# Kernel optimization log

Hardware: AMD Instinct MI355X
Metric: run time of the kernel (lower is better)

## Reference

```python
import jax, jax.numpy as jnp
import numpy as np

WS = 8        # world_size (tp group size)
M = 8192      # global M, divisible by WS
N = 4096
LOCAL_K = 1024  # K // WS


def setup_inputs() -> dict:
    key = jax.random.key(0)
    k1, k2 = jax.random.split(key)
    # Per-rank K-sharded activation and weight (transpose_weight=False => weight is [N, local_K])
    inp = jax.random.normal(k1, (WS, M, LOCAL_K), dtype=jnp.float32)
    wgt = jax.random.normal(k2, (WS, N, LOCAL_K), dtype=jnp.float32) * 0.02
    return {"input": inp, "weight": wgt}


def reference(input, weight):
    """GEMM + reduce-scatter across the TP group.

    Each rank r computes partial_r = input[r] @ weight[r].T  -> [M, N].
    Reduce: full = sum_r partial_r. Scatter: rank r receives rows
    [r*M/WS : (r+1)*M/WS]. We return the scattered result for all ranks
    stacked on the leading axis: [WS, M//WS, N].
    """
    # Contract over both the rank axis (the reduce) and local_K in one einsum.
    full = jnp.einsum('rmk,rnk->mn', input, weight)  # [M, N]
    return full.reshape(WS, M // WS, N)
```

## Files before the change

### kernel.cpp

```cpp
#include <hip/hip_runtime.h>
#include <hip/hip_bf16.h>


#define M_TOT 8192
#define N_TOT 4096
#define LK    1024
#define NR    8
#define K_TOT (NR * LK)
#define NT    (K_TOT / 64)

typedef float f32x4 __attribute__((ext_vector_type(4)));
typedef short s16x8 __attribute__((ext_vector_type(8)));
typedef const __attribute__((address_space(1))) unsigned int* gptr_t;
typedef __attribute__((address_space(3))) unsigned int* lptr_t;

__device__ inline short f2bf(float f) {
    __hip_bfloat16 h = __float2bfloat16(f);
    return *reinterpret_cast<short*>(&h);
}

__global__ __launch_bounds__(256)
void cvt_bf16(const float* __restrict__ in, short* __restrict__ out,
              int row_shift, int row_mask) {
    const int row = blockIdx.x * 2 + (threadIdx.x >> 7);
    const int c   = (threadIdx.x & 127) * 8;
    const int r   = row >> row_shift;
    const int m   = row & row_mask;
    const float* src = in + ((size_t)row << 10) + c;
    f32x4 v0 = *(const f32x4*)src;
    f32x4 v1 = *(const f32x4*)(src + 4);
    s16x8 o;
    #pragma unroll
    for (int j = 0; j < 4; ++j) { o[j] = f2bf(v0[j]); o[j + 4] = f2bf(v1[j]); }
    *(s16x8*)(out + ((size_t)m << 13) + ((size_t)r << 10) + c) = o;
}


__device__ __forceinline__ void stage_half(const short* srcBase, short* ldsOp,
                                           int half, int ktile, int wid) {
    #pragma unroll
    for (int q = 0; q < 2; ++q) {
        const short* src = srcBase + (size_t)(half * 128 + q * 8) * K_TOT + ktile * 64;
        short* dst = ldsOp + (half * 128 + wid * 16 + q * 8) * 64;
        __builtin_amdgcn_global_load_lds((gptr_t)src, (lptr_t)dst, 16, 0, 0);
    }
}

template<int C>
__device__ __forceinline__ void read_a_pair(s16x8 (&afr)[8][2], const short* lAc,
                                            int wm, int r15, int kg) {
    #pragma unroll
    for (int fo = 0; fo < 2; ++fo)
        #pragma unroll
        for (int ks = 0; ks < 2; ++ks) {
            const int row = C * 64 + wm * 32 + fo * 16 + r15;
            const int off = row * 64 + ((((ks << 2) | kg) ^ (row & 7)) << 3);
            afr[C * 2 + fo][ks] = *(const s16x8*)(lAc + off);
        }
}

__device__ __forceinline__ void read_b(s16x8 (&bfr)[4][2], const short* lBc,
                                       int wn, int r15, int kg) {
    #pragma unroll
    for (int n = 0; n < 4; ++n)
        #pragma unroll
        for (int ks = 0; ks < 2; ++ks) {
            const int row = wn * 64 + n * 16 + r15;
            const int off = row * 64 + ((((ks << 2) | kg) ^ (row & 7)) << 3);
            bfr[n][ks] = *(const s16x8*)(lBc + off);
        }
}

template<int Q>
__device__ __forceinline__ void mfma_quad(f32x4 (&acc)[8][4], s16x8 (&afr)[8][2],
                                          s16x8 (&bfr)[4][2]) {
    __builtin_amdgcn_s_setprio(1);
    #pragma unroll
    for (int fo = 0; fo < 2; ++fo)
        #pragma unroll
        for (int n = 0; n < 4; ++n)
            #pragma unroll
            for (int ks = 0; ks < 2; ++ks)
                acc[Q * 2 + fo][n] = __builtin_amdgcn_mfma_f32_16x16x32_bf16(
                    afr[Q * 2 + fo][ks], bfr[n][ks], acc[Q * 2 + fo][n], 0, 0, 0);
    __builtin_amdgcn_s_setprio(0);
}

#define MEMCLOB asm volatile("" ::: "memory")
#define BAR     __builtin_amdgcn_s_barrier()
#define SCHED0  __builtin_amdgcn_sched_barrier(0)

#define TILE_BODY(P) do {                                                     \
    const int t = 2 * t2 + (P);                                               \
    const short* lAc = smem + ((P) << 15);                                    \
    short* bufN = smem + (((P) ^ 1) << 15);                                   \
    short* bufC = smem + ((P) << 15);                                         \
                                             \
    read_a_pair<1>(afr, lAc, wm, r15, kg);                                    \
    if (t + 1 < NT) stage_half(srcA, bufN, 1, t + 1, wid);                    \
    MEMCLOB; BAR;                                                             \
    asm volatile("s_waitcnt lgkmcnt(4)" ::: "memory"); SCHED0;                \
    mfma_quad<0>(acc, afr, bfr);                                              \
    MEMCLOB; BAR;                                                             \
         \
    read_a_pair<2>(afr, lAc, wm, r15, kg);                                    \
    if (t + 2 < NT) stage_half(srcB, bufC + 16384, 0, t + 2, wid);            \
    MEMCLOB; BAR;                                                             \
    asm volatile("s_waitcnt lgkmcnt(4)" ::: "memory"); SCHED0;                \
    mfma_quad<1>(acc, afr, bfr);                                              \
    MEMCLOB; BAR;                                                             \
                                             \
    read_a_pair<3>(afr, lAc, wm, r15, kg);                                    \
    if (t + 2 < NT) stage_half(srcB, bufC + 16384, 1, t + 2, wid);            \
    MEMCLOB; BAR;                                                             \
    asm volatile("s_waitcnt lgkmcnt(4)" ::: "memory"); SCHED0;                \
    mfma_quad<2>(acc, afr, bfr);                                              \
    MEMCLOB; BAR;                                                             \
    \
    \
    \
    \
    asm volatile("s_waitcnt lgkmcnt(0)" ::: "memory");                        \
    if (t < NT - 2)       asm volatile("s_waitcnt vmcnt(4)" ::: "memory");    \
    else if (t == NT - 2) asm volatile("s_waitcnt vmcnt(0)" ::: "memory");    \
    MEMCLOB; BAR; SCHED0;                                                     \
    mfma_quad<3>(acc, afr, bfr);                                              \
    if (t + 1 < NT) {                                                         \
        read_b(bfr, bufN + 16384, wn, r15, kg);                               \
        read_a_pair<0>(afr, bufN, wm, r15, kg);                               \
    }                                                                         \
    if (t + 2 < NT) stage_half(srcA, bufC, 0, t + 2, wid);                    \
    MEMCLOB; BAR;                                                             \
} while (0)

__global__ __launch_bounds__(512, 2)
void gemm8(const short* __restrict__ A, const short* __restrict__ B,
           float* __restrict__ C) {
    extern __shared__ short smem[];

    const int tid  = threadIdx.x;
    const int lane = tid & 63;
    const int wid  = tid >> 6;
    const int wm   = wid >> 2;
    const int wn   = wid & 3;
    const int r15  = lane & 15;
    const int kg   = lane >> 4;
    const int l8   = lane >> 3;
    const int g16  = (lane & 7) ^ l8;

    const int bid = blockIdx.x;
    const int sw  = (bid & 7) * 64 + (bid >> 3);
    const int bm  = sw >> 4;
    const int bn  = sw & 15;

    const short* srcA = A + (size_t)(bm * 256 + wid * 16 + l8) * K_TOT + g16 * 8;
    const short* srcB = B + (size_t)(bn * 256 + wid * 16 + l8) * K_TOT + g16 * 8;

    stage_half(srcB, smem + 16384, 0, 0, wid);
    stage_half(srcB, smem + 16384, 1, 0, wid);
    stage_half(srcA, smem,         0, 0, wid);
    stage_half(srcA, smem,         1, 0, wid);
    stage_half(srcB, smem + 49152, 0, 1, wid);
    stage_half(srcB, smem + 49152, 1, 1, wid);
    stage_half(srcA, smem + 32768, 0, 1, wid);
    asm volatile("s_waitcnt vmcnt(6)" ::: "memory");
    MEMCLOB; BAR;

    f32x4 acc[8][4];
    #pragma unroll
    for (int f = 0; f < 8; ++f)
        #pragma unroll
        for (int n = 0; n < 4; ++n)
            acc[f][n] = (f32x4){0.f, 0.f, 0.f, 0.f};

    s16x8 afr[8][2];
    s16x8 bfr[4][2];

    read_b(bfr, smem + 16384, wn, r15, kg);
    read_a_pair<0>(afr, smem, wm, r15, kg);

    for (int t2 = 0; t2 < NT / 2; ++t2) {
        TILE_BODY(0);
        TILE_BODY(1);
    }

    float* Cp = C + (size_t)(bm * 256 + wm * 32 + kg * 4) * N_TOT
                  + bn * 256 + wn * 64 + r15;
    #pragma unroll
    for (int f = 0; f < 8; ++f)
        #pragma unroll
        for (int n = 0; n < 4; ++n)
            #pragma unroll
            for (int jj = 0; jj < 4; ++jj) {
                const int roff = (f >> 1) * 64 + (f & 1) * 16 + jj;
                Cp[(size_t)roff * N_TOT + n * 16] = acc[f][n][jj];
            }
}

#define PAD_ROW 40
__global__ __launch_bounds__(256, 2)
void gemm_rs_fused(const float* __restrict__ A, const float* __restrict__ B,
                   float* __restrict__ C) {
    __shared__ short lA[128 * PAD_ROW];
    __shared__ short lB[128 * PAD_ROW];
    const int bid = blockIdx.x;
    const int sw  = (bid & 7) * (int)(gridDim.x >> 3) + (bid >> 3);
    const int bm = sw >> 5, bn = sw & 31;
    const int tid = threadIdx.x, lane = tid & 63, wid = tid >> 6;
    const int wr = wid >> 1, wc = wid & 1, r15 = lane & 15, kg = lane >> 4;
    const int srow = tid >> 1, scg = tid & 1;
    const float* gA = A + ((size_t)(bm * 128 + srow) << 10) + scg * 16;
    const float* gB = B + ((size_t)(bn * 128 + srow) << 10) + scg * 16;
    short* wpA = lA + srow * PAD_ROW + scg * 16;
    short* wpB = lB + srow * PAD_ROW + scg * 16;
    const short* rpA = lA + (wr * 64 + r15) * PAD_ROW + kg * 8;
    const short* rpB = lB + (wc * 64 + r15) * PAD_ROW + kg * 8;
    f32x4 acc[4][4];
    #pragma unroll
    for (int i = 0; i < 4; ++i)
        #pragma unroll
        for (int j = 0; j < 4; ++j) acc[i][j] = (f32x4){0.f, 0.f, 0.f, 0.f};
    for (int t = 0; t < K_TOT / 32; ++t) {
        const int r = t >> 5, k0 = (t & 31) << 5;
        const float* pA = gA + (size_t)r * (M_TOT * LK) + k0;
        const float* pB = gB + (size_t)r * (N_TOT * LK) + k0;
        f32x4 va[4], vb[4];
        #pragma unroll
        for (int q = 0; q < 4; ++q) va[q] = *(const f32x4*)(pA + q * 4);
        #pragma unroll
        for (int q = 0; q < 4; ++q) vb[q] = *(const f32x4*)(pB + q * 4);
        __syncthreads();
        s16x8 oa0, oa1, ob0, ob1;
        #pragma unroll
        for (int q = 0; q < 2; ++q)
            #pragma unroll
            for (int i = 0; i < 4; ++i) {
                oa0[q * 4 + i] = f2bf(va[q][i]);
                oa1[q * 4 + i] = f2bf(va[q + 2][i]);
                ob0[q * 4 + i] = f2bf(vb[q][i]);
                ob1[q * 4 + i] = f2bf(vb[q + 2][i]);
            }
        *(s16x8*)(wpA) = oa0; *(s16x8*)(wpA + 8) = oa1;
        *(s16x8*)(wpB) = ob0; *(s16x8*)(wpB + 8) = ob1;
        __syncthreads();
        s16x8 af[4], bfr2[4];
        #pragma unroll
        for (int i = 0; i < 4; ++i) af[i]   = *(const s16x8*)(rpA + i * 16 * PAD_ROW);
        #pragma unroll
        for (int i = 0; i < 4; ++i) bfr2[i] = *(const s16x8*)(rpB + i * 16 * PAD_ROW);
        #pragma unroll
        for (int i = 0; i < 4; ++i)
            #pragma unroll
            for (int j = 0; j < 4; ++j)
                acc[i][j] = __builtin_amdgcn_mfma_f32_16x16x32_bf16(
                    af[i], bfr2[j], acc[i][j], 0, 0, 0);
    }
    float* Cp = C + (size_t)(bm * 128 + wr * 64 + kg * 4) * N_TOT
                  + bn * 128 + wc * 64 + r15;
    #pragma unroll
    for (int i = 0; i < 4; ++i)
        #pragma unroll
        for (int j = 0; j < 4; ++j)
            #pragma unroll
            for (int jj = 0; jj < 4; ++jj)
                Cp[(size_t)(i * 16 + jj) * N_TOT + j * 16] = acc[i][j][jj];
}

extern "C" void kernel_launch(void* const* d_in, const int* in_sizes, int n_in,
                              void* d_out, int out_size, void* d_ws, size_t ws_size,
                              hipStream_t stream) {
    const float* A = (const float*)d_in[0];
    const float* B = (const float*)d_in[1];
    float* C = (float*)d_out;

    const size_t needA = (size_t)M_TOT * K_TOT * 2;
    const size_t needB = (size_t)N_TOT * K_TOT * 2;

    if (ws_size >= needA + needB) {
        short* Abf = (short*)d_ws;
        short* Bbf = (short*)((char*)d_ws + needA);
        cvt_bf16<<<dim3(NR * M_TOT / 2), dim3(256), 0, stream>>>(A, Abf, 13, 8191);
        cvt_bf16<<<dim3(NR * N_TOT / 2), dim3(256), 0, stream>>>(B, Bbf, 12, 4095);
        gemm8<<<dim3((M_TOT / 256) * (N_TOT / 256)), dim3(512), 131072, stream>>>(Abf, Bbf, C);
    } else {
        gemm_rs_fused<<<dim3((M_TOT / 128) * (N_TOT / 128)), dim3(256), 0, stream>>>(A, B, C);
    }
}
```

Baseline: 523.4 us.

## Replace ping-pong tile macro with simple double-buffered K loop

Removes the hand-interleaved two-tile TILE_BODY schedule, which spread global-to-LDS staging across sub-phases with many barriers. In its place is a plain loop: wait for all loads, one barrier, read fragments, issue the whole next tile's prefetch, then run four MFMA quads with partial LDS waits. The A-fragment register array shrinks to two slots and launch bounds drop to one block per CU, freeing registers. This cuts barrier count and code complexity, but the full vmcnt(0) wait each iteration limits how much global latency overlaps with compute.

```diff
diff --git a/kernel.cpp b/kernel.cpp
--- a/kernel.cpp
+++ b/kernel.cpp
@@ -47,7 +47,7 @@
 }
 
 template<int C>
-__device__ __forceinline__ void read_a_pair(s16x8 (&afr)[8][2], const short* lAc,
+__device__ __forceinline__ void read_a_pair(s16x8 (&afr)[2][2][2], const short* lAc,
                                             int wm, int r15, int kg) {
     #pragma unroll
     for (int fo = 0; fo < 2; ++fo)
@@ -55,7 +55,7 @@
         for (int ks = 0; ks < 2; ++ks) {
             const int row = C * 64 + wm * 32 + fo * 16 + r15;
             const int off = row * 64 + ((((ks << 2) | kg) ^ (row & 7)) << 3);
-            afr[C * 2 + fo][ks] = *(const s16x8*)(lAc + off);
+            afr[C & 1][fo][ks] = *(const s16x8*)(lAc + off);
         }
 }
 
@@ -72,7 +72,7 @@
 }
 
 template<int Q>
-__device__ __forceinline__ void mfma_quad(f32x4 (&acc)[8][4], s16x8 (&afr)[8][2],
+__device__ __forceinline__ void mfma_quad(f32x4 (&acc)[8][4], s16x8 (&afr)[2][2][2],
                                           s16x8 (&bfr)[4][2]) {
     __builtin_amdgcn_s_setprio(1);
     #pragma unroll
@@ -82,7 +82,7 @@
             #pragma unroll
             for (int ks = 0; ks < 2; ++ks)
                 acc[Q * 2 + fo][n] = __builtin_amdgcn_mfma_f32_16x16x32_bf16(
-                    afr[Q * 2 + fo][ks], bfr[n][ks], acc[Q * 2 + fo][n], 0, 0, 0);
+                    afr[Q & 1][fo][ks], bfr[n][ks], acc[Q * 2 + fo][n], 0, 0, 0);
     __builtin_amdgcn_s_setprio(0);
 }
 
@@ -90,50 +90,7 @@
 #define BAR     __builtin_amdgcn_s_barrier()
 #define SCHED0  __builtin_amdgcn_sched_barrier(0)
 
-#define TILE_BODY(P) do {                                                     \
-    const int t = 2 * t2 + (P);                                               \
-    const short* lAc = smem + ((P) << 15);                                    \
-    short* bufN = smem + (((P) ^ 1) << 15);                                   \
-    short* bufC = smem + ((P) << 15);                                         \
-                                             \
-    read_a_pair<1>(afr, lAc, wm, r15, kg);                                    \
-    if (t + 1 < NT) stage_half(srcA, bufN, 1, t + 1, wid);                    \
-    MEMCLOB; BAR;                                                             \
-    asm volatile("s_waitcnt lgkmcnt(4)" ::: "memory"); SCHED0;                \
-    mfma_quad<0>(acc, afr, bfr);                                              \
-    MEMCLOB; BAR;                                                             \
-         \
-    read_a_pair<2>(afr, lAc, wm, r15, kg);                                    \
-    if (t + 2 < NT) stage_half(srcB, bufC + 16384, 0, t + 2, wid);            \
-    MEMCLOB; BAR;                                                             \
-    asm volatile("s_waitcnt lgkmcnt(4)" ::: "memory"); SCHED0;                \
-    mfma_quad<1>(acc, afr, bfr);                                              \
-    MEMCLOB; BAR;                                                             \
-                                             \
-    read_a_pair<3>(afr, lAc, wm, r15, kg);                                    \
-    if (t + 2 < NT) stage_half(srcB, bufC + 16384, 1, t + 2, wid);            \
-    MEMCLOB; BAR;                                                             \
-    asm volatile("s_waitcnt lgkmcnt(4)" ::: "memory"); SCHED0;                \
-    mfma_quad<2>(acc, afr, bfr);                                              \
-    MEMCLOB; BAR;                                                             \
-    \
-    \
-    \
-    \
-    asm volatile("s_waitcnt lgkmcnt(0)" ::: "memory");                        \
-    if (t < NT - 2)       asm volatile("s_waitcnt vmcnt(4)" ::: "memory");    \
-    else if (t == NT - 2) asm volatile("s_waitcnt vmcnt(0)" ::: "memory");    \
-    MEMCLOB; BAR; SCHED0;                                                     \
-    mfma_quad<3>(acc, afr, bfr);                                              \
-    if (t + 1 < NT) {                                                         \
-        read_b(bfr, bufN + 16384, wn, r15, kg);                               \
-        read_a_pair<0>(afr, bufN, wm, r15, kg);                               \
-    }                                                                         \
-    if (t + 2 < NT) stage_half(srcA, bufC, 0, t + 2, wid);                    \
-    MEMCLOB; BAR;                                                             \
-} while (0)
-
-__global__ __launch_bounds__(512, 2)
+__global__ __launch_bounds__(512, 1)
 void gemm8(const short* __restrict__ A, const short* __restrict__ B,
            float* __restrict__ C) {
     extern __shared__ short smem[];
@@ -160,11 +117,6 @@
     stage_half(srcB, smem + 16384, 1, 0, wid);
     stage_half(srcA, smem,         0, 0, wid);
     stage_half(srcA, smem,         1, 0, wid);
-    stage_half(srcB, smem + 49152, 0, 1, wid);
-    stage_half(srcB, smem + 49152, 1, 1, wid);
-    stage_half(srcA, smem + 32768, 0, 1, wid);
-    asm volatile("s_waitcnt vmcnt(6)" ::: "memory");
-    MEMCLOB; BAR;
 
     f32x4 acc[8][4];
     #pragma unroll
@@ -173,15 +125,39 @@
         for (int n = 0; n < 4; ++n)
             acc[f][n] = (f32x4){0.f, 0.f, 0.f, 0.f};
 
-    s16x8 afr[8][2];
+    s16x8 afr[2][2][2];
     s16x8 bfr[4][2];
 
-    read_b(bfr, smem + 16384, wn, r15, kg);
-    read_a_pair<0>(afr, smem, wm, r15, kg);
-
-    for (int t2 = 0; t2 < NT / 2; ++t2) {
-        TILE_BODY(0);
-        TILE_BODY(1);
+    for (int t = 0; t < NT; ++t) {
+        const int par = t & 1;
+        const short* bufC = smem + (par << 15);
+        short* bufN = smem + ((par ^ 1) << 15);
+
+        asm volatile("s_waitcnt vmcnt(0)" ::: "memory");
+        MEMCLOB; BAR;
+
+        read_b(bfr, bufC + 16384, wn, r15, kg);
+        read_a_pair<0>(afr, bufC, wm, r15, kg);
+        read_a_pair<1>(afr, bufC, wm, r15, kg);
+
+        if (t + 1 < NT) {
+            stage_half(srcB, bufN + 16384, 0, t + 1, wid);
+            stage_half(srcB, bufN + 16384, 1, t + 1, wid);
+            stage_half(srcA, bufN,         0, t + 1, wid);
+            stage_half(srcA, bufN,         1, t + 1, wid);
+        }
+
+        asm volatile("s_waitcnt lgkmcnt(4)" ::: "memory"); SCHED0;
+        mfma_quad<0>(acc, afr, bfr);
+        read_a_pair<2>(afr, bufC, wm, r15, kg);
+        asm volatile("s_waitcnt lgkmcnt(4)" ::: "memory"); SCHED0;
+        mfma_quad<1>(acc, afr, bfr);
+        read_a_pair<3>(afr, bufC, wm, r15, kg);
+        asm volatile("s_waitcnt lgkmcnt(4)" ::: "memory"); SCHED0;
+        mfma_quad<2>(acc, afr, bfr);
+        asm volatile("s_waitcnt lgkmcnt(0)" ::: "memory"); SCHED0;
+        mfma_quad<3>(acc, afr, bfr);
+        MEMCLOB;
     }
 
     float* Cp = C + (size_t)(bm * 256 + wm * 32 + kg * 4) * N_TOT
```

After: 571.5 us. +9.2%, slower.

## Interleave next-tile B fragment loads with last MFMA quad and precompute LDS addresses

Applied to the files above, without the earlier changes.

Merges the two fp32-to-bf16 conversion launches into a single launch. In the GEMM it precomputes the swizzled LDS read pointers and the per-wave staging pointers, shrinks the A-fragment register array from [8][2] to a double-buffered [2][2][2], and advances the global pointers incrementally. The final MFMA quad of each tile is split per N-column so the next tile's B fragments load right after each column's MFMAs. The A stage for tile t+2 is also issued earlier. The goal is to hide LDS read latency behind MFMA work, cut address arithmetic, and lower register pressure. The trade-off is tighter reliance on hand-placed waitcnt counts and barrier ordering, which could stall or become incorrect if miscounted.

```diff
diff --git a/kernel.cpp b/kernel.cpp
--- a/kernel.cpp
+++ b/kernel.cpp
@@ -20,9 +20,15 @@
 }
 
 __global__ __launch_bounds__(256)
-void cvt_bf16(const float* __restrict__ in, short* __restrict__ out,
-              int row_shift, int row_mask) {
-    const int row = blockIdx.x * 2 + (threadIdx.x >> 7);
+void cvt_all(const float* __restrict__ A, const float* __restrict__ B,
+             short* __restrict__ Abf, short* __restrict__ Bbf) {
+    int bid = blockIdx.x;
+    const float* in;
+    short* out;
+    int row_shift, row_mask;
+    if (bid < 32768) { in = A; out = Abf; row_shift = 13; row_mask = 8191; }
+    else { bid -= 32768; in = B; out = Bbf; row_shift = 12; row_mask = 4095; }
+    const int row = bid * 2 + (threadIdx.x >> 7);
     const int c   = (threadIdx.x & 127) * 8;
     const int r   = row >> row_shift;
     const int m   = row & row_mask;
@@ -36,43 +42,46 @@
 }
 
 
-__device__ __forceinline__ void stage_half(const short* srcBase, short* ldsOp,
-                                           int half, int ktile, int wid) {
+template<int HALF, int D>
+__device__ __forceinline__ void stage(const short* g, short* l) {
     #pragma unroll
     for (int q = 0; q < 2; ++q) {
-        const short* src = srcBase + (size_t)(half * 128 + q * 8) * K_TOT + ktile * 64;
-        short* dst = ldsOp + (half * 128 + wid * 16 + q * 8) * 64;
+        const short* src = g + (size_t)(HALF * 128 + q * 8) * K_TOT + D * 64;
+        short* dst = l + (HALF * 128 + q * 8) * 64;
         __builtin_amdgcn_global_load_lds((gptr_t)src, (lptr_t)dst, 16, 0, 0);
     }
 }
 
 template<int C>
-__device__ __forceinline__ void read_a_pair(s16x8 (&afr)[8][2], const short* lAc,
-                                            int wm, int r15, int kg) {
+__device__ __forceinline__ void read_a(s16x8 (&afr)[2][2][2],
+                                       const short* bA0, const short* bA1) {
     #pragma unroll
     for (int fo = 0; fo < 2; ++fo)
         #pragma unroll
-        for (int ks = 0; ks < 2; ++ks) {
-            const int row = C * 64 + wm * 32 + fo * 16 + r15;
-            const int off = row * 64 + ((((ks << 2) | kg) ^ (row & 7)) << 3);
-            afr[C * 2 + fo][ks] = *(const s16x8*)(lAc + off);
-        }
-}
-
-__device__ __forceinline__ void read_b(s16x8 (&bfr)[4][2], const short* lBc,
-                                       int wn, int r15, int kg) {
+        for (int ks = 0; ks < 2; ++ks)
+            afr[C & 1][fo][ks] =
+                *(const s16x8*)((ks ? bA1 : bA0) + (C * 64 + fo * 16) * 64);
+}
+
+__device__ __forceinline__ void read_b(s16x8 (&bfr)[4][2],
+                                       const short* bB0, const short* bB1) {
     #pragma unroll
     for (int n = 0; n < 4; ++n)
         #pragma unroll
-        for (int ks = 0; ks < 2; ++ks) {
-            const int row = wn * 64 + n * 16 + r15;
-            const int off = row * 64 + ((((ks << 2) | kg) ^ (row & 7)) << 3);
-            bfr[n][ks] = *(const s16x8*)(lBc + off);
-        }
+        for (int ks = 0; ks < 2; ++ks)
+            bfr[n][ks] = *(const s16x8*)((ks ? bB1 : bB0) + n * 1024);
+}
+
+template<int N>
+__device__ __forceinline__ void read_b_one(s16x8 (&bfr)[4][2],
+                                           const short* bB0, const short* bB1) {
+    #pragma unroll
+    for (int ks = 0; ks < 2; ++ks)
+        bfr[N][ks] = *(const s16x8*)((ks ? bB1 : bB0) + N * 1024);
 }
 
 template<int Q>
-__device__ __forceinline__ void mfma_quad(f32x4 (&acc)[8][4], s16x8 (&afr)[8][2],
+__device__ __forceinline__ void mfma_quad(f32x4 (&acc)[8][4], s16x8 (&afr)[2][2][2],
                                           s16x8 (&bfr)[4][2]) {
     __builtin_amdgcn_s_setprio(1);
     #pragma unroll
@@ -82,55 +91,74 @@
             #pragma unroll
             for (int ks = 0; ks < 2; ++ks)
                 acc[Q * 2 + fo][n] = __builtin_amdgcn_mfma_f32_16x16x32_bf16(
-                    afr[Q * 2 + fo][ks], bfr[n][ks], acc[Q * 2 + fo][n], 0, 0, 0);
+                    afr[Q & 1][fo][ks], bfr[n][ks], acc[Q * 2 + fo][n], 0, 0, 0);
     __builtin_amdgcn_s_setprio(0);
+}
+
+template<int N>
+__device__ __forceinline__ void mfma_n3(f32x4 (&acc)[8][4], s16x8 (&afr)[2][2][2],
+                                        s16x8 (&bfr)[4][2]) {
+    #pragma unroll
+    for (int fo = 0; fo < 2; ++fo)
+        #pragma unroll
+        for (int ks = 0; ks < 2; ++ks)
+            acc[6 + fo][N] = __builtin_amdgcn_mfma_f32_16x16x32_bf16(
+                afr[1][fo][ks], bfr[N][ks], acc[6 + fo][N], 0, 0, 0);
 }
 
 #define MEMCLOB asm volatile("" ::: "memory")
 #define BAR     __builtin_amdgcn_s_barrier()
 #define SCHED0  __builtin_amdgcn_sched_barrier(0)
 
+#define INTERLEAVE_STEP(N, PP) do {                                           \
+    mfma_n3<N>(acc, afr, bfr);                                                \
+    read_b_one<N>(bfr, bB0[(PP) ^ 1], bB1[(PP) ^ 1]); } while (0)
+
 #define TILE_BODY(P) do {                                                     \
     const int t = 2 * t2 + (P);                                               \
-    const short* lAc = smem + ((P) << 15);                                    \
-    short* bufN = smem + (((P) ^ 1) << 15);                                   \
-    short* bufC = smem + ((P) << 15);                                         \
                                              \
-    read_a_pair<1>(afr, lAc, wm, r15, kg);                                    \
-    if (t + 1 < NT) stage_half(srcA, bufN, 1, t + 1, wid);                    \
+    read_a<1>(afr, bA0[P], bA1[P]);                                           \
+    if (t + 1 < NT) stage<1, 1>(gA, stA[(P) ^ 1]);                            \
     MEMCLOB; BAR;                                                             \
     asm volatile("s_waitcnt lgkmcnt(4)" ::: "memory"); SCHED0;                \
     mfma_quad<0>(acc, afr, bfr);                                              \
     MEMCLOB; BAR;                                                             \
-         \
-    read_a_pair<2>(afr, lAc, wm, r15, kg);                                    \
-    if (t + 2 < NT) stage_half(srcB, bufC + 16384, 0, t + 2, wid);            \
+                                             \
+    read_a<2>(afr, bA0[P], bA1[P]);                                           \
+    if (t + 2 < NT) stage<0, 2>(gB, stB[P]);                                  \
     MEMCLOB; BAR;                                                             \
     asm volatile("s_waitcnt lgkmcnt(4)" ::: "memory"); SCHED0;                \
     mfma_quad<1>(acc, afr, bfr);                                              \
     MEMCLOB; BAR;                                                             \
                                              \
-    read_a_pair<3>(afr, lAc, wm, r15, kg);                                    \
-    if (t + 2 < NT) stage_half(srcB, bufC + 16384, 1, t + 2, wid);            \
+    read_a<3>(afr, bA0[P], bA1[P]);                                           \
+    if (t + 2 < NT) stage<1, 2>(gB, stB[P]);                                  \
     MEMCLOB; BAR;                                                             \
     asm volatile("s_waitcnt lgkmcnt(4)" ::: "memory"); SCHED0;                \
     mfma_quad<2>(acc, afr, bfr);                                              \
     MEMCLOB; BAR;                                                             \
     \
     \
-    \
-    \
-    asm volatile("s_waitcnt lgkmcnt(0)" ::: "memory");                        \
     if (t < NT - 2)       asm volatile("s_waitcnt vmcnt(4)" ::: "memory");    \
     else if (t == NT - 2) asm volatile("s_waitcnt vmcnt(0)" ::: "memory");    \
-    MEMCLOB; BAR; SCHED0;                                                     \
-    mfma_quad<3>(acc, afr, bfr);                                              \
+    MEMCLOB; BAR;                                                             \
+    if (t + 2 < NT) stage<0, 2>(gA, stA[P]);                                  \
     if (t + 1 < NT) {                                                         \
-        read_b(bfr, bufN + 16384, wn, r15, kg);                               \
-        read_a_pair<0>(afr, bufN, wm, r15, kg);                               \
+        read_a<0>(afr, bA0[(P) ^ 1], bA1[(P) ^ 1]);                           \
+        asm volatile("s_waitcnt lgkmcnt(4)" ::: "memory"); SCHED0;            \
+        __builtin_amdgcn_s_setprio(1);                                        \
+        INTERLEAVE_STEP(0, P); INTERLEAVE_STEP(1, P);                         \
+        INTERLEAVE_STEP(2, P); INTERLEAVE_STEP(3, P);                         \
+        __builtin_amdgcn_s_setprio(0);                                        \
+    } else {                                                                  \
+        asm volatile("s_waitcnt lgkmcnt(0)" ::: "memory"); SCHED0;            \
+        __builtin_amdgcn_s_setprio(1);                                        \
+        mfma_n3<0>(acc, afr, bfr); mfma_n3<1>(acc, afr, bfr);                 \
+        mfma_n3<2>(acc, afr, bfr); mfma_n3<3>(acc, afr, bfr);                 \
+        __builtin_amdgcn_s_setprio(0);                                        \
     }                                                                         \
-    if (t + 2 < NT) stage_half(srcA, bufC, 0, t + 2, wid);                    \
-    MEMCLOB; BAR;                                                             \
+    MEMCLOB; BAR;                                                             \
+    gA += 64; gB += 64;                                                       \
 } while (0)
 
 __global__ __launch_bounds__(512, 2)
@@ -147,22 +175,38 @@
     const int kg   = lane >> 4;
     const int l8   = lane >> 3;
     const int g16  = (lane & 7) ^ l8;
+    const int r7   = r15 & 7;
 
     const int bid = blockIdx.x;
     const int sw  = (bid & 7) * 64 + (bid >> 3);
     const int bm  = sw >> 4;
     const int bn  = sw & 15;
 
-    const short* srcA = A + (size_t)(bm * 256 + wid * 16 + l8) * K_TOT + g16 * 8;
-    const short* srcB = B + (size_t)(bn * 256 + wid * 16 + l8) * K_TOT + g16 * 8;
-
-    stage_half(srcB, smem + 16384, 0, 0, wid);
-    stage_half(srcB, smem + 16384, 1, 0, wid);
-    stage_half(srcA, smem,         0, 0, wid);
-    stage_half(srcA, smem,         1, 0, wid);
-    stage_half(srcB, smem + 49152, 0, 1, wid);
-    stage_half(srcB, smem + 49152, 1, 1, wid);
-    stage_half(srcA, smem + 32768, 0, 1, wid);
+    const short* gA = A + (size_t)(bm * 256 + wid * 16 + l8) * K_TOT + g16 * 8;
+    const short* gB = B + (size_t)(bn * 256 + wid * 16 + l8) * K_TOT + g16 * 8;
+
+    short* stA[2] = { smem + wid * 1024, smem + 32768 + wid * 1024 };
+    short* stB[2] = { smem + 16384 + wid * 1024, smem + 49152 + wid * 1024 };
+
+    const int gk0 = kg ^ r7;
+    const int gk1 = (4 | kg) ^ r7;
+    const short* bA0[2], *bA1[2], *bB0[2], *bB1[2];
+    #pragma unroll
+    for (int p = 0; p < 2; ++p) {
+        const short* base = smem + p * 32768;
+        bA0[p] = base + (wm * 32 + r15) * 64 + gk0 * 8;
+        bA1[p] = base + (wm * 32 + r15) * 64 + gk1 * 8;
+        bB0[p] = base + 16384 + (wn * 64 + r15) * 64 + gk0 * 8;
+        bB1[p] = base + 16384 + (wn * 64 + r15) * 64 + gk1 * 8;
+    }
+
+    stage<0, 0>(gB, stB[0]);
+    stage<1, 0>(gB, stB[0]);
+    stage<0, 0>(gA, stA[0]);
+    stage<1, 0>(gA, stA[0]);
+    stage<0, 1>(gB, stB[1]);
+    stage<1, 1>(gB, stB[1]);
+    stage<0, 1>(gA, stA[1]);
     asm volatile("s_waitcnt vmcnt(6)" ::: "memory");
     MEMCLOB; BAR;
 
@@ -173,11 +217,11 @@
         for (int n = 0; n < 4; ++n)
             acc[f][n] = (f32x4){0.f, 0.f, 0.f, 0.f};
 
-    s16x8 afr[8][2];
+    s16x8 afr[2][2][2];
     s16x8 bfr[4][2];
 
-    read_b(bfr, smem + 16384, wn, r15, kg);
-    read_a_pair<0>(afr, smem, wm, r15, kg);
+    read_b(bfr, bB0[0], bB1[0]);
+    read_a<0>(afr, bA0[0], bA1[0]);
 
     for (int t2 = 0; t2 < NT / 2; ++t2) {
         TILE_BODY(0);
@@ -279,8 +323,7 @@
     if (ws_size >= needA + needB) {
         short* Abf = (short*)d_ws;
         short* Bbf = (short*)((char*)d_ws + needA);
-        cvt_bf16<<<dim3(NR * M_TOT / 2), dim3(256), 0, stream>>>(A, Abf, 13, 8191);
-        cvt_bf16<<<dim3(NR * N_TOT / 2), dim3(256), 0, stream>>>(B, Bbf, 12, 4095);
+        cvt_all<<<dim3(NR * (M_TOT + N_TOT) / 2), dim3(256), 0, stream>>>(A, B, Abf, Bbf);
         gemm8<<<dim3((M_TOT / 256) * (N_TOT / 256)), dim3(512), 131072, stream>>>(Abf, Bbf, C);
     } else {
         gemm_rs_fused<<<dim3((M_TOT / 128) * (N_TOT / 128)), dim3(256), 0, stream>>>(A, B, C);
```

Measured after the change: 519.2 us. Within noise of the previous version (-0.8%).

## Restructure bf16 GEMM to 32-wide K tiles with interleaved MFMA/LDS pipeline

Applied to the files above, without the earlier changes.

The main GEMM now uses K tiles of 32 instead of 64, halving LDS use to 64 KB. It gives each wave a 128x64 output footprint with a new XOR swizzle and interleaves the B-fragment LDS reads for the next tile with the current tile's MFMA columns. The two fp32-to-bf16 conversion launches are merged into one kernel. The aim is better overlap of LDS reads, global-to-LDS staging and MFMA work, plus more occupancy headroom and one fewer launch. The cost is twice as many loop iterations and barriers per K step, and a more fragile waitcnt schedule.

```diff
diff --git a/kernel.cpp b/kernel.cpp
--- a/kernel.cpp
+++ b/kernel.cpp
@@ -7,7 +7,7 @@
 #define LK    1024
 #define NR    8
 #define K_TOT (NR * LK)
-#define NT    (K_TOT / 64)
+#define NT32  (K_TOT / 32)
 
 typedef float f32x4 __attribute__((ext_vector_type(4)));
 typedef short s16x8 __attribute__((ext_vector_type(8)));
@@ -20,9 +20,15 @@
 }
 
 __global__ __launch_bounds__(256)
-void cvt_bf16(const float* __restrict__ in, short* __restrict__ out,
-              int row_shift, int row_mask) {
-    const int row = blockIdx.x * 2 + (threadIdx.x >> 7);
+void cvt_all(const float* __restrict__ A, const float* __restrict__ B,
+             short* __restrict__ Abf, short* __restrict__ Bbf) {
+    int bid = blockIdx.x;
+    const float* in;
+    short* out;
+    int row_shift, row_mask;
+    if (bid < 32768) { in = A; out = Abf; row_shift = 13; row_mask = 8191; }
+    else { bid -= 32768; in = B; out = Bbf; row_shift = 12; row_mask = 4095; }
+    const int row = bid * 2 + (threadIdx.x >> 7);
     const int c   = (threadIdx.x & 127) * 8;
     const int r   = row >> row_shift;
     const int m   = row & row_mask;
@@ -36,106 +42,98 @@
 }
 
 
-__device__ __forceinline__ void stage_half(const short* srcBase, short* ldsOp,
-                                           int half, int ktile, int wid) {
-    #pragma unroll
-    for (int q = 0; q < 2; ++q) {
-        const short* src = srcBase + (size_t)(half * 128 + q * 8) * K_TOT + ktile * 64;
-        short* dst = ldsOp + (half * 128 + wid * 16 + q * 8) * 64;
-        __builtin_amdgcn_global_load_lds((gptr_t)src, (lptr_t)dst, 16, 0, 0);
-    }
-}
-
-template<int C>
-__device__ __forceinline__ void read_a_pair(s16x8 (&afr)[8][2], const short* lAc,
-                                            int wm, int r15, int kg) {
-    #pragma unroll
-    for (int fo = 0; fo < 2; ++fo)
-        #pragma unroll
-        for (int ks = 0; ks < 2; ++ks) {
-            const int row = C * 64 + wm * 32 + fo * 16 + r15;
-            const int off = row * 64 + ((((ks << 2) | kg) ^ (row & 7)) << 3);
-            afr[C * 2 + fo][ks] = *(const s16x8*)(lAc + off);
-        }
-}
-
-__device__ __forceinline__ void read_b(s16x8 (&bfr)[4][2], const short* lBc,
-                                       int wn, int r15, int kg) {
+__device__ __forceinline__ void stage2(const short* g, short* l) {
+    #pragma unroll
+    for (int q = 0; q < 2; ++q)
+        __builtin_amdgcn_global_load_lds((gptr_t)(g + (size_t)q * 128 * K_TOT),
+                                         (lptr_t)(l + q * 4096), 16, 0, 0);
+}
+
+template<int F0>
+__device__ __forceinline__ void read_a4(s16x8 (&a)[8], const short* pA) {
+    #pragma unroll
+    for (int i = 0; i < 4; ++i)
+        a[F0 + i] = *(const s16x8*)(pA + (F0 + i) * 512);
+}
+
+__device__ __forceinline__ void read_b4(s16x8 (&b)[4], const short* pB) {
     #pragma unroll
     for (int n = 0; n < 4; ++n)
-        #pragma unroll
-        for (int ks = 0; ks < 2; ++ks) {
-            const int row = wn * 64 + n * 16 + r15;
-            const int off = row * 64 + ((((ks << 2) | kg) ^ (row & 7)) << 3);
-            bfr[n][ks] = *(const s16x8*)(lBc + off);
-        }
-}
-
-template<int Q>
-__device__ __forceinline__ void mfma_quad(f32x4 (&acc)[8][4], s16x8 (&afr)[8][2],
-                                          s16x8 (&bfr)[4][2]) {
-    __builtin_amdgcn_s_setprio(1);
-    #pragma unroll
-    for (int fo = 0; fo < 2; ++fo)
+        b[n] = *(const s16x8*)(pB + n * 512);
+}
+
+template<int N>
+__device__ __forceinline__ void read_b1(s16x8 (&b)[4], const short* pB) {
+    b[N] = *(const s16x8*)(pB + N * 512);
+}
+
+template<int F0>
+__device__ __forceinline__ void mfma_half(f32x4 (&acc)[8][4], s16x8 (&a)[8],
+                                          s16x8 (&b)[4]) {
+    #pragma unroll
+    for (int f = 0; f < 4; ++f)
         #pragma unroll
         for (int n = 0; n < 4; ++n)
-            #pragma unroll
-            for (int ks = 0; ks < 2; ++ks)
-                acc[Q * 2 + fo][n] = __builtin_amdgcn_mfma_f32_16x16x32_bf16(
-                    afr[Q * 2 + fo][ks], bfr[n][ks], acc[Q * 2 + fo][n], 0, 0, 0);
-    __builtin_amdgcn_s_setprio(0);
+            acc[F0 + f][n] = __builtin_amdgcn_mfma_f32_16x16x32_bf16(
+                a[F0 + f], b[n], acc[F0 + f][n], 0, 0, 0);
+}
+
+template<int N>
+__device__ __forceinline__ void mfma_col(f32x4 (&acc)[8][4], s16x8 (&a)[8],
+                                         s16x8 (&b)[4]) {
+    #pragma unroll
+    for (int f = 4; f < 8; ++f)
+        acc[f][N] = __builtin_amdgcn_mfma_f32_16x16x32_bf16(
+            a[f], b[N], acc[f][N], 0, 0, 0);
 }
 
 #define MEMCLOB asm volatile("" ::: "memory")
 #define BAR     __builtin_amdgcn_s_barrier()
 #define SCHED0  __builtin_amdgcn_sched_barrier(0)
 
+#define ILV(N, PP) do {                                                       \
+    mfma_col<N>(acc, a, b);                                                   \
+    read_b1<N>(b, bB[(PP) ^ 1]); } while (0)
+
 #define TILE_BODY(P) do {                                                     \
     const int t = 2 * t2 + (P);                                               \
-    const short* lAc = smem + ((P) << 15);                                    \
-    short* bufN = smem + (((P) ^ 1) << 15);                                   \
-    short* bufC = smem + ((P) << 15);                                         \
-                                             \
-    read_a_pair<1>(afr, lAc, wm, r15, kg);                                    \
-    if (t + 1 < NT) stage_half(srcA, bufN, 1, t + 1, wid);                    \
+    \
+    \
+    read_a4<4>(a, bA[P]);                                                     \
+    MEMCLOB;                                                                  \
+    asm volatile("s_waitcnt lgkmcnt(4)" ::: "memory"); SCHED0;                \
     MEMCLOB; BAR;                                                             \
-    asm volatile("s_waitcnt lgkmcnt(4)" ::: "memory"); SCHED0;                \
-    mfma_quad<0>(acc, afr, bfr);                                              \
+    if (t < NT32 - 2) stage2(gB + 64, sB[P]);                                 \
+    __builtin_amdgcn_s_setprio(1);                                            \
+    mfma_half<0>(acc, a, b);                                                  \
+    __builtin_amdgcn_s_setprio(0);                                            \
+    \
+    \
+    MEMCLOB;                                                                  \
+    asm volatile("s_waitcnt lgkmcnt(0)" ::: "memory"); SCHED0;                \
     MEMCLOB; BAR;                                                             \
-         \
-    read_a_pair<2>(afr, lAc, wm, r15, kg);                                    \
-    if (t + 2 < NT) stage_half(srcB, bufC + 16384, 0, t + 2, wid);            \
+    if (t < NT32 - 2) stage2(gA + 64, sA[P]);                                 \
+    if (t < NT32 - 2)       asm volatile("s_waitcnt vmcnt(4)" ::: "memory");  \
+    else if (t == NT32 - 2) asm volatile("s_waitcnt vmcnt(0)" ::: "memory");  \
     MEMCLOB; BAR;                                                             \
-    asm volatile("s_waitcnt lgkmcnt(4)" ::: "memory"); SCHED0;                \
-    mfma_quad<1>(acc, afr, bfr);                                              \
-    MEMCLOB; BAR;                                                             \
-                                             \
-    read_a_pair<3>(afr, lAc, wm, r15, kg);                                    \
-    if (t + 2 < NT) stage_half(srcB, bufC + 16384, 1, t + 2, wid);            \
-    MEMCLOB; BAR;                                                             \
-    asm volatile("s_waitcnt lgkmcnt(4)" ::: "memory"); SCHED0;                \
-    mfma_quad<2>(acc, afr, bfr);                                              \
-    MEMCLOB; BAR;                                                             \
-    \
-    \
-    \
-    \
-    asm volatile("s_waitcnt lgkmcnt(0)" ::: "memory");                        \
-    if (t < NT - 2)       asm volatile("s_waitcnt vmcnt(4)" ::: "memory");    \
-    else if (t == NT - 2) asm volatile("s_waitcnt vmcnt(0)" ::: "memory");    \
-    MEMCLOB; BAR; SCHED0;                                                     \
-    mfma_quad<3>(acc, afr, bfr);                                              \
-    if (t + 1 < NT) {                                                         \
-        read_b(bfr, bufN + 16384, wn, r15, kg);                               \
-        read_a_pair<0>(afr, bufN, wm, r15, kg);                               \
+    if (t + 1 < NT32) {                                                       \
+        __builtin_amdgcn_s_setprio(1);                                        \
+        ILV(0, P); ILV(1, P); ILV(2, P); ILV(3, P);                           \
+        read_a4<0>(a, bA[(P) ^ 1]);                                           \
+        __builtin_amdgcn_s_setprio(0);                                        \
+    } else {                                                                  \
+        __builtin_amdgcn_s_setprio(1);                                        \
+        mfma_col<0>(acc, a, b); mfma_col<1>(acc, a, b);                       \
+        mfma_col<2>(acc, a, b); mfma_col<3>(acc, a, b);                       \
+        __builtin_amdgcn_s_setprio(0);                                        \
     }                                                                         \
-    if (t + 2 < NT) stage_half(srcA, bufC, 0, t + 2, wid);                    \
-    MEMCLOB; BAR;                                                             \
+    MEMCLOB;                                                                  \
+    gA += 32; gB += 32;                                                       \
 } while (0)
 
 __global__ __launch_bounds__(512, 2)
-void gemm8(const short* __restrict__ A, const short* __restrict__ B,
-           float* __restrict__ C) {
+void gemm32(const short* __restrict__ A, const short* __restrict__ B,
+            float* __restrict__ C) {
     extern __shared__ short smem[];
 
     const int tid  = threadIdx.x;
@@ -145,25 +143,31 @@
     const int wn   = wid & 3;
     const int r15  = lane & 15;
     const int kg   = lane >> 4;
-    const int l8   = lane >> 3;
-    const int g16  = (lane & 7) ^ l8;
+    const int l4   = lane >> 2;
+    const int g4   = (lane & 3) ^ (l4 & 3);
 
     const int bid = blockIdx.x;
     const int sw  = (bid & 7) * 64 + (bid >> 3);
     const int bm  = sw >> 4;
     const int bn  = sw & 15;
 
-    const short* srcA = A + (size_t)(bm * 256 + wid * 16 + l8) * K_TOT + g16 * 8;
-    const short* srcB = B + (size_t)(bn * 256 + wid * 16 + l8) * K_TOT + g16 * 8;
-
-    stage_half(srcB, smem + 16384, 0, 0, wid);
-    stage_half(srcB, smem + 16384, 1, 0, wid);
-    stage_half(srcA, smem,         0, 0, wid);
-    stage_half(srcA, smem,         1, 0, wid);
-    stage_half(srcB, smem + 49152, 0, 1, wid);
-    stage_half(srcB, smem + 49152, 1, 1, wid);
-    stage_half(srcA, smem + 32768, 0, 1, wid);
-    asm volatile("s_waitcnt vmcnt(6)" ::: "memory");
+    const short* gA = A + (size_t)(bm * 256 + wid * 16 + l4) * K_TOT + g4 * 8;
+    const short* gB = B + (size_t)(bn * 256 + wid * 16 + l4) * K_TOT + g4 * 8;
+
+    short* sA[2] = { smem + wid * 512, smem + 16384 + wid * 512 };
+    short* sB[2] = { smem + 8192 + wid * 512, smem + 24576 + wid * 512 };
+
+    const int rbase = r15 * 32 + ((kg ^ (r15 & 3)) << 3);
+    const short* bA[2] = { smem + wm * 4096 + rbase,
+                           smem + 16384 + wm * 4096 + rbase };
+    const short* bB[2] = { smem + 8192 + wn * 2048 + rbase,
+                           smem + 24576 + wn * 2048 + rbase };
+
+    stage2(gB, sB[0]);
+    stage2(gA, sA[0]);
+    stage2(gB + 32, sB[1]);
+    stage2(gA + 32, sA[1]);
+    asm volatile("s_waitcnt vmcnt(4)" ::: "memory");
     MEMCLOB; BAR;
 
     f32x4 acc[8][4];
@@ -173,28 +177,26 @@
         for (int n = 0; n < 4; ++n)
             acc[f][n] = (f32x4){0.f, 0.f, 0.f, 0.f};
 
-    s16x8 afr[8][2];
-    s16x8 bfr[4][2];
-
-    read_b(bfr, smem + 16384, wn, r15, kg);
-    read_a_pair<0>(afr, smem, wm, r15, kg);
-
-    for (int t2 = 0; t2 < NT / 2; ++t2) {
+    s16x8 a[8];
+    s16x8 b[4];
+
+    read_b4(b, bB[0]);
+    read_a4<0>(a, bA[0]);
+
+    for (int t2 = 0; t2 < NT32 / 2; ++t2) {
         TILE_BODY(0);
         TILE_BODY(1);
     }
 
-    float* Cp = C + (size_t)(bm * 256 + wm * 32 + kg * 4) * N_TOT
+    float* Cp = C + (size_t)(bm * 256 + wm * 128 + kg * 4) * N_TOT
                   + bn * 256 + wn * 64 + r15;
     #pragma unroll
     for (int f = 0; f < 8; ++f)
         #pragma unroll
         for (int n = 0; n < 4; ++n)
             #pragma unroll
-            for (int jj = 0; jj < 4; ++jj) {
-                const int roff = (f >> 1) * 64 + (f & 1) * 16 + jj;
-                Cp[(size_t)roff * N_TOT + n * 16] = acc[f][n][jj];
-            }
+            for (int jj = 0; jj < 4; ++jj)
+                Cp[(size_t)(f * 16 + jj) * N_TOT + n * 16] = acc[f][n][jj];
 }
 
 #define PAD_ROW 40
@@ -279,9 +281,8 @@
     if (ws_size >= needA + needB) {
         short* Abf = (short*)d_ws;
         short* Bbf = (short*)((char*)d_ws + needA);
-        cvt_bf16<<<dim3(NR * M_TOT / 2), dim3(256), 0, stream>>>(A, Abf, 13, 8191);
-        cvt_bf16<<<dim3(NR * N_TOT / 2), dim3(256), 0, stream>>>(B, Bbf, 12, 4095);
-        gemm8<<<dim3((M_TOT / 256) * (N_TOT / 256)), dim3(512), 131072, stream>>>(Abf, Bbf, C);
+        cvt_all<<<dim3(NR * (M_TOT + N_TOT) / 2), dim3(256), 0, stream>>>(A, B, Abf, Bbf);
+        gemm32<<<dim3((M_TOT / 256) * (N_TOT / 256)), dim3(512), 65536, stream>>>(Abf, Bbf, C);
     } else {
         gemm_rs_fused<<<dim3((M_TOT / 128) * (N_TOT / 128)), dim3(256), 0, stream>>>(A, B, C);
     }
```

New measurement: 602.8 us. 15.2% more time.
